# Performance work log

Measured on AMD Instinct MI355X. Metric: run time of the kernel, lower is better.

The kernel has to match this reference:

```python
import jax, jax.numpy as jnp
import numpy as np

LOSS_WEIGHT = 1.0
BIG = 1e9  # finite sentinel for masked-out pixels (avoids inf-grad NaNs)


def setup_inputs() -> dict:
    key = jax.random.key(0)
    k1, k2 = jax.random.split(key)
    B, N, H, W = 4, 6890, 64, 64
    vert2d = jax.random.uniform(k1, (B, N, 2), dtype=jnp.float32) * jnp.array([W, H], jnp.float32)
    mask = jax.random.randint(k2, (B, H, W), 0, 2, dtype=jnp.int32)
    return {"vert2d": vert2d, "mask": mask}


def reference(vert2d, mask):
    B, N, _ = vert2d.shape
    _, H, W = mask.shape
    scale = jnp.array([W, H], vert2d.dtype)
    v = vert2d / scale  # [B,N,2], normalized
    # all pixel coords as (x, y), normalized -- the dense equivalent of torch.where points
    ys, xs = jnp.meshgrid(jnp.arange(H), jnp.arange(W), indexing="ij")
    pts = (jnp.stack([xs.ravel(), ys.ravel()], axis=-1).astype(v.dtype) / scale)  # [HW,2]
    valid = (mask.reshape(B, -1) > 0)  # [B,HW] boolean membership of each pixel
    # pairwise L2 distances: [B,N,HW]
    diff = v[:, :, None, :] - pts[None, None, :, :]
    d = jnp.sqrt(jnp.sum(diff * diff, axis=-1))
    dm = jnp.where(valid[:, None, :], d, BIG)
    # sum over mask points of min over verts  +  sum over verts of min over mask points
    loss = jnp.sum(jnp.min(dm, axis=1) * valid) + jnp.sum(jnp.min(dm, axis=2))
    return LOSS_WEIGHT * loss
```

## Files before the change

### kernel.cpp

```cpp
#include <hip/hip_runtime.h>

#define NB 4
#define NV 6890
#define HW 4096
#define NPAD 6912
#define T1_CS 108
#define T1_BLOCKS 1024
#define T2_BLOCKS 896
#define NRED_BLOCKS 172

#define OFF_VT   0
#define OFF_PL   442368
#define OFF_T1   704512
#define OFF_T2   770048
#define OFF_PART 880640

#define FLT_MAX_BITS 0x7F7FFFFFu
#define FINF 3.402823466e38f
#define PBIG 1.0e18f

__global__ __launch_bounds__(256) void k_prep(const float* __restrict__ vert,
                                              const int* __restrict__ mask,
                                              float4* __restrict__ vt,
                                              float4* __restrict__ pl,
                                              unsigned* __restrict__ t1,
                                              unsigned* __restrict__ t2) {
    int gid = blockIdx.x * 256 + threadIdx.x;
    t2[gid] = FLT_MAX_BITS;
    int b = gid / NPAD, n = gid - b * NPAD;
    if (n < NV) {
        float2 v = reinterpret_cast<const float2*>(vert)[b * NV + n];
        vt[gid] = make_float4(-2.f * v.x, -2.f * v.y, fmaf(v.x, v.x, v.y * v.y), 0.f);
    } else {
        vt[gid] = make_float4(0.f, 0.f, PBIG, 0.f);
    }
    if (gid < NB * HW) {
        t1[gid] = FLT_MAX_BITS;
        float fx = (float)(gid & 63), fy = (float)((gid >> 6) & 63);
        float pz = (mask[gid] > 0) ? fmaf(fx, fx, fy * fy) : PBIG;
        pl[gid] = make_float4(-2.f * fx, -2.f * fy, pz, 0.f);
    }
}

__global__ __launch_bounds__(256) void k_main(const float* __restrict__ vert,
                                              const float4* __restrict__ vt,
                                              const float4* __restrict__ pl,
                                              unsigned* __restrict__ t1,
                                              unsigned* __restrict__ t2) {
    __shared__ float4 lds[128];
    int bx = blockIdx.x, tid = threadIdx.x;
    if (bx < T1_BLOCKS) {
        int c = bx & 63, q = (bx >> 6) & 3, b = bx >> 8;
        if (tid < T1_CS) lds[tid] = vt[b * NPAD + c * T1_CS + tid];
        __syncthreads();
        int x = tid & 63, ry = tid >> 6;
        float fx = (float)x;
        float fy0 = (float)(q * 16 + ry);
        float fy1 = fy0 + 4.f, fy2 = fy0 + 8.f, fy3 = fy0 + 12.f;
        float m0 = FINF, m1 = FINF, m2 = FINF, m3 = FINF;
        #pragma unroll 4
        for (int i = 0; i < T1_CS; i += 2) {
            float4 a = lds[i], g = lds[i + 1];
            float ta = fmaf(a.x, fx, a.z);
            float tg = fmaf(g.x, fx, g.z);
            m0 = fminf(m0, fminf(fmaf(a.y, fy0, ta), fmaf(g.y, fy0, tg)));
            m1 = fminf(m1, fminf(fmaf(a.y, fy1, ta), fmaf(g.y, fy1, tg)));
            m2 = fminf(m2, fminf(fmaf(a.y, fy2, ta), fmaf(g.y, fy2, tg)));
            m3 = fminf(m3, fminf(fmaf(a.y, fy3, ta), fmaf(g.y, fy3, tg)));
        }
        float fx2 = fx * fx;
        int y0 = q * 16 + ry;
        unsigned* tp = t1 + (b << 12) + x;
        m0 = fmaxf(fmaf(fy0, fy0, fx2) + m0, 0.f);
        m1 = fmaxf(fmaf(fy1, fy1, fx2) + m1, 0.f);
        m2 = fmaxf(fmaf(fy2, fy2, fx2) + m2, 0.f);
        m3 = fmaxf(fmaf(fy3, fy3, fx2) + m3, 0.f);
        atomicMin(tp + (y0     ) * 64, __float_as_uint(m0));
        atomicMin(tp + (y0 +  4) * 64, __float_as_uint(m1));
        atomicMin(tp + (y0 +  8) * 64, __float_as_uint(m2));
        atomicMin(tp + (y0 + 12) * 64, __float_as_uint(m3));
    } else {
        int t2i = bx - T1_BLOCKS;
        int pc = t2i & 31;
        int r  = t2i >> 5;
        int g  = r % 7, b = r / 7;
        if (tid < 128) lds[tid] = pl[b * HW + pc * 128 + tid];
        __syncthreads();
        int n0 = g * 1024 + tid;
        const float2* vv = reinterpret_cast<const float2*>(vert) + b * NV;
        float vx[4], vy[4];
        bool  val[4];
        #pragma unroll
        for (int k = 0; k < 4; ++k) {
            int n = n0 + 256 * k;
            val[k] = (n < NV);
            float2 t = val[k] ? vv[n] : make_float2(0.f, 0.f);
            vx[k] = t.x; vy[k] = t.y;
        }
        float mm[4] = {FINF, FINF, FINF, FINF};
        #pragma unroll 4
        for (int j = 0; j < 128; j += 2) {
            float4 a = lds[j], cc = lds[j + 1];
            #pragma unroll
            for (int k = 0; k < 4; ++k) {
                float da = fmaf(a.x,  vx[k], fmaf(a.y,  vy[k], a.z));
                float dc = fmaf(cc.x, vx[k], fmaf(cc.y, vy[k], cc.z));
                mm[k] = fminf(mm[k], fminf(da, dc));
            }
        }
        #pragma unroll
        for (int k = 0; k < 4; ++k) {
            if (val[k]) {
                float m = fmaxf(mm[k] + fmaf(vx[k], vx[k], vy[k] * vy[k]), 0.f);
                atomicMin(&t2[b * NPAD + n0 + 256 * k], __float_as_uint(m));
            }
        }
    }
}

__global__ __launch_bounds__(256) void k_red1(const unsigned* __restrict__ t1,
                                              const unsigned* __restrict__ t2,
                                              const int* __restrict__ mask,
                                              float* __restrict__ part) {
    int gid = blockIdx.x * 256 + threadIdx.x;
    float v = 0.f;
    if (gid < HW * NB) {
        if (mask[gid] > 0)
            v = sqrtf(__uint_as_float(t1[gid])) * (1.0f / 64.0f);
    } else {
        int j = gid - HW * NB;
        int bb = j / NPAD;
        int n  = j - bb * NPAD;
        if (n < NV)
            v = sqrtf(__uint_as_float(t2[j])) * (1.0f / 64.0f);
    }
    __shared__ float sbuf[4];
    for (int off = 32; off; off >>= 1) v += __shfl_down(v, off, 64);
    int lane = threadIdx.x & 63, wid = threadIdx.x >> 6;
    if (!lane) sbuf[wid] = v;
    __syncthreads();
    if (wid == 0) {
        v = (lane < 4) ? sbuf[lane] : 0.f;
        v += __shfl_down(v, 2, 64);
        v += __shfl_down(v, 1, 64);
        if (!lane) part[blockIdx.x] = v;
    }
}

__global__ __launch_bounds__(256) void k_red2(const float* __restrict__ part,
                                              float* __restrict__ out) {
    float v = (threadIdx.x < NRED_BLOCKS) ? part[threadIdx.x] : 0.f;
    __shared__ float sbuf[4];
    for (int off = 32; off; off >>= 1) v += __shfl_down(v, off, 64);
    int lane = threadIdx.x & 63, wid = threadIdx.x >> 6;
    if (!lane) sbuf[wid] = v;
    __syncthreads();
    if (threadIdx.x == 0) out[0] = sbuf[0] + sbuf[1] + sbuf[2] + sbuf[3];
}

extern "C" void kernel_launch(void* const* d_in, const int* in_sizes, int n_in,
                              void* d_out, int out_size, void* d_ws, size_t ws_size,
                              hipStream_t stream) {
    const float* vert = (const float*)d_in[0];
    const int*   mask = (const int*)d_in[1];
    char* ws = (char*)d_ws;
    float4*   vt  = (float4*)(ws + OFF_VT);
    float4*   pl  = (float4*)(ws + OFF_PL);
    unsigned* t1  = (unsigned*)(ws + OFF_T1);
    unsigned* t2  = (unsigned*)(ws + OFF_T2);
    float*    prt = (float*)(ws + OFF_PART);
    float*    out = (float*)d_out;

    k_prep<<<108, 256, 0, stream>>>(vert, mask, vt, pl, t1, t2);
    k_main<<<T1_BLOCKS + T2_BLOCKS, 256, 0, stream>>>(vert, vt, pl, t1, t2);
    k_red1<<<NRED_BLOCKS, 256, 0, stream>>>(t1, t2, mask, prt);
    k_red2<<<1, 256, 0, stream>>>(prt, out);
}
```

Baseline: 76.04 us.

## Fuse prep into main kernel, replace atomics with partial buffers, single-pass reduction

Removes the separate prep kernel by computing the vertex and pixel LDS tiles inside the main kernel, and doubles the per-block chunk sizes. Cross-block atomicMin is replaced by writing per-chunk partial minima to large scratch buffers, which the reduction kernel then min-reduces. The final sum uses an atomicAdd with a ticket counter so the second reduction kernel is no longer needed. This cuts two launches and the atomic contention, at the cost of more global memory traffic for the partial buffers and fewer blocks in the main kernel.

```diff
diff --git a/kernel.cpp b/kernel.cpp
--- a/kernel.cpp
+++ b/kernel.cpp
@@ -4,87 +4,75 @@
 #define NV 6890
 #define HW 4096
 #define NPAD 6912
-#define T1_CS 108
-#define T1_BLOCKS 1024
-#define T2_BLOCKS 896
+#define C1 32
+#define T1CS 216
+#define C2 16
+#define T1_BLOCKS 512
+#define T2_BLOCKS 448
 #define NRED_BLOCKS 172
 
-#define OFF_VT   0
-#define OFF_PL   442368
-#define OFF_T1   704512
-#define OFF_T2   770048
-#define OFF_PART 880640
+#define OFF_T1P 0
+#define OFF_T2P 2097152
+#define OFF_SUM 3866624
+#define OFF_TKT 3866628
 
-#define FLT_MAX_BITS 0x7F7FFFFFu
 #define FINF 3.402823466e38f
 #define PBIG 1.0e18f
 
-__global__ __launch_bounds__(256) void k_prep(const float* __restrict__ vert,
+__global__ __launch_bounds__(256) void k_main(const float* __restrict__ vert,
                                               const int* __restrict__ mask,
-                                              float4* __restrict__ vt,
-                                              float4* __restrict__ pl,
-                                              unsigned* __restrict__ t1,
-                                              unsigned* __restrict__ t2) {
-    int gid = blockIdx.x * 256 + threadIdx.x;
-    t2[gid] = FLT_MAX_BITS;
-    int b = gid / NPAD, n = gid - b * NPAD;
-    if (n < NV) {
-        float2 v = reinterpret_cast<const float2*>(vert)[b * NV + n];
-        vt[gid] = make_float4(-2.f * v.x, -2.f * v.y, fmaf(v.x, v.x, v.y * v.y), 0.f);
-    } else {
-        vt[gid] = make_float4(0.f, 0.f, PBIG, 0.f);
-    }
-    if (gid < NB * HW) {
-        t1[gid] = FLT_MAX_BITS;
-        float fx = (float)(gid & 63), fy = (float)((gid >> 6) & 63);
-        float pz = (mask[gid] > 0) ? fmaf(fx, fx, fy * fy) : PBIG;
-        pl[gid] = make_float4(-2.f * fx, -2.f * fy, pz, 0.f);
-    }
-}
-
-__global__ __launch_bounds__(256) void k_main(const float* __restrict__ vert,
-                                              const float4* __restrict__ vt,
-                                              const float4* __restrict__ pl,
-                                              unsigned* __restrict__ t1,
-                                              unsigned* __restrict__ t2) {
-    __shared__ float4 lds[128];
+                                              float* __restrict__ t1p,
+                                              float* __restrict__ t2p,
+                                              float* __restrict__ sum,
+                                              unsigned* __restrict__ tkt) {
+    __shared__ float4 lds[256];
     int bx = blockIdx.x, tid = threadIdx.x;
+    if (bx == 0 && tid == 0) { *sum = 0.f; *tkt = 0u; }
     if (bx < T1_BLOCKS) {
-        int c = bx & 63, q = (bx >> 6) & 3, b = bx >> 8;
-        if (tid < T1_CS) lds[tid] = vt[b * NPAD + c * T1_CS + tid];
+        int c = bx & 31, q = (bx >> 5) & 3, b = bx >> 7;
+        if (tid < T1CS) {
+            int n = c * T1CS + tid;
+            float4 w = make_float4(0.f, 0.f, PBIG, 0.f);
+            if (n < NV) {
+                float2 v = reinterpret_cast<const float2*>(vert)[b * NV + n];
+                w = make_float4(-2.f * v.x, -2.f * v.y, fmaf(v.x, v.x, v.y * v.y), 0.f);
+            }
+            lds[tid] = w;
+        }
         __syncthreads();
         int x = tid & 63, ry = tid >> 6;
-        float fx = (float)x;
+        float fx  = (float)x;
         float fy0 = (float)(q * 16 + ry);
         float fy1 = fy0 + 4.f, fy2 = fy0 + 8.f, fy3 = fy0 + 12.f;
         float m0 = FINF, m1 = FINF, m2 = FINF, m3 = FINF;
         #pragma unroll 4
-        for (int i = 0; i < T1_CS; i += 2) {
-            float4 a = lds[i], g = lds[i + 1];
-            float ta = fmaf(a.x, fx, a.z);
-            float tg = fmaf(g.x, fx, g.z);
-            m0 = fminf(m0, fminf(fmaf(a.y, fy0, ta), fmaf(g.y, fy0, tg)));
-            m1 = fminf(m1, fminf(fmaf(a.y, fy1, ta), fmaf(g.y, fy1, tg)));
-            m2 = fminf(m2, fminf(fmaf(a.y, fy2, ta), fmaf(g.y, fy2, tg)));
-            m3 = fminf(m3, fminf(fmaf(a.y, fy3, ta), fmaf(g.y, fy3, tg)));
+        for (int i = 0; i < T1CS; i += 2) {
+            float4 a = lds[i], g2 = lds[i + 1];
+            float ta = fmaf(a.x,  fx, a.z);
+            float tg = fmaf(g2.x, fx, g2.z);
+            m0 = fminf(m0, fminf(fmaf(a.y, fy0, ta), fmaf(g2.y, fy0, tg)));
+            m1 = fminf(m1, fminf(fmaf(a.y, fy1, ta), fmaf(g2.y, fy1, tg)));
+            m2 = fminf(m2, fminf(fmaf(a.y, fy2, ta), fmaf(g2.y, fy2, tg)));
+            m3 = fminf(m3, fminf(fmaf(a.y, fy3, ta), fmaf(g2.y, fy3, tg)));
         }
         float fx2 = fx * fx;
         int y0 = q * 16 + ry;
-        unsigned* tp = t1 + (b << 12) + x;
-        m0 = fmaxf(fmaf(fy0, fy0, fx2) + m0, 0.f);
-        m1 = fmaxf(fmaf(fy1, fy1, fx2) + m1, 0.f);
-        m2 = fmaxf(fmaf(fy2, fy2, fx2) + m2, 0.f);
-        m3 = fmaxf(fmaf(fy3, fy3, fx2) + m3, 0.f);
-        atomicMin(tp + (y0     ) * 64, __float_as_uint(m0));
-        atomicMin(tp + (y0 +  4) * 64, __float_as_uint(m1));
-        atomicMin(tp + (y0 +  8) * 64, __float_as_uint(m2));
-        atomicMin(tp + (y0 + 12) * 64, __float_as_uint(m3));
+        float* tp = t1p + ((c * NB + b) << 12) + x;
+        tp[(y0     ) * 64] = fmaf(fy0, fy0, fx2) + m0;
+        tp[(y0 +  4) * 64] = fmaf(fy1, fy1, fx2) + m1;
+        tp[(y0 +  8) * 64] = fmaf(fy2, fy2, fx2) + m2;
+        tp[(y0 + 12) * 64] = fmaf(fy3, fy3, fx2) + m3;
     } else {
         int t2i = bx - T1_BLOCKS;
-        int pc = t2i & 31;
-        int r  = t2i >> 5;
+        int pc = t2i & 15;
+        int r  = t2i >> 4;
         int g  = r % 7, b = r / 7;
-        if (tid < 128) lds[tid] = pl[b * HW + pc * 128 + tid];
+        {
+            int pix = pc * 256 + tid;
+            float fx = (float)(pix & 63), fy = (float)(pix >> 6);
+            float pz = (mask[b * HW + pix] > 0) ? fmaf(fx, fx, fy * fy) : PBIG;
+            lds[tid] = make_float4(-2.f * fx, -2.f * fy, pz, 0.f);
+        }
         __syncthreads();
         int n0 = g * 1024 + tid;
         const float2* vv = reinterpret_cast<const float2*>(vert) + b * NV;
@@ -98,8 +86,8 @@
             vx[k] = t.x; vy[k] = t.y;
         }
         float mm[4] = {FINF, FINF, FINF, FINF};
-        #pragma unroll 4
-        for (int j = 0; j < 128; j += 2) {
+        #pragma unroll 2
+        for (int j = 0; j < 256; j += 2) {
             float4 a = lds[j], cc = lds[j + 1];
             #pragma unroll
             for (int k = 0; k < 4; ++k) {
@@ -108,54 +96,55 @@
                 mm[k] = fminf(mm[k], fminf(da, dc));
             }
         }
+        float* op = t2p + pc * (NB * NPAD) + b * NPAD + n0;
         #pragma unroll
-        for (int k = 0; k < 4; ++k) {
-            if (val[k]) {
-                float m = fmaxf(mm[k] + fmaf(vx[k], vx[k], vy[k] * vy[k]), 0.f);
-                atomicMin(&t2[b * NPAD + n0 + 256 * k], __float_as_uint(m));
-            }
-        }
+        for (int k = 0; k < 4; ++k)
+            if (val[k]) op[256 * k] = mm[k] + fmaf(vx[k], vx[k], vy[k] * vy[k]);
     }
 }
 
-__global__ __launch_bounds__(256) void k_red1(const unsigned* __restrict__ t1,
-                                              const unsigned* __restrict__ t2,
-                                              const int* __restrict__ mask,
-                                              float* __restrict__ part) {
+__global__ __launch_bounds__(256) void k_red(const float* __restrict__ t1p,
+                                             const float* __restrict__ t2p,
+                                             const int* __restrict__ mask,
+                                             float* __restrict__ sum,
+                                             unsigned* __restrict__ tkt,
+                                             float* __restrict__ out) {
     int gid = blockIdx.x * 256 + threadIdx.x;
     float v = 0.f;
-    if (gid < HW * NB) {
-        if (mask[gid] > 0)
-            v = sqrtf(__uint_as_float(t1[gid])) * (1.0f / 64.0f);
+    if (gid < NB * HW) {
+        if (mask[gid] > 0) {
+            float m = FINF;
+            #pragma unroll
+            for (int c = 0; c < C1; ++c) m = fminf(m, t1p[c * (NB * HW) + gid]);
+            v = sqrtf(fmaxf(m, 0.f)) * (1.0f / 64.0f);
+        }
     } else {
-        int j = gid - HW * NB;
-        int bb = j / NPAD;
-        int n  = j - bb * NPAD;
-        if (n < NV)
-            v = sqrtf(__uint_as_float(t2[j])) * (1.0f / 64.0f);
+        int j = gid - NB * HW;
+        int b = j / NPAD;
+        int n = j - b * NPAD;
+        if (n < NV) {
+            float m = FINF;
+            #pragma unroll
+            for (int pc = 0; pc < C2; ++pc) m = fminf(m, t2p[pc * (NB * NPAD) + j]);
+            v = sqrtf(fmaxf(m, 0.f)) * (1.0f / 64.0f);
+        }
     }
     __shared__ float sbuf[4];
+    __shared__ bool last;
     for (int off = 32; off; off >>= 1) v += __shfl_down(v, off, 64);
     int lane = threadIdx.x & 63, wid = threadIdx.x >> 6;
     if (!lane) sbuf[wid] = v;
     __syncthreads();
-    if (wid == 0) {
-        v = (lane < 4) ? sbuf[lane] : 0.f;
-        v += __shfl_down(v, 2, 64);
-        v += __shfl_down(v, 1, 64);
-        if (!lane) part[blockIdx.x] = v;
+    if (threadIdx.x == 0) {
+        float bs = sbuf[0] + sbuf[1] + sbuf[2] + sbuf[3];
+        atomicAdd(sum, bs);
+        __threadfence();
+        unsigned t = atomicAdd(tkt, 1u);
+        last = (t == NRED_BLOCKS - 1);
     }
-}
-
-__global__ __launch_bounds__(256) void k_red2(const float* __restrict__ part,
-                                              float* __restrict__ out) {
-    float v = (threadIdx.x < NRED_BLOCKS) ? part[threadIdx.x] : 0.f;
-    __shared__ float sbuf[4];
-    for (int off = 32; off; off >>= 1) v += __shfl_down(v, off, 64);
-    int lane = threadIdx.x & 63, wid = threadIdx.x >> 6;
-    if (!lane) sbuf[wid] = v;
     __syncthreads();
-    if (threadIdx.x == 0) out[0] = sbuf[0] + sbuf[1] + sbuf[2] + sbuf[3];
+    if (last && threadIdx.x == 0)
+        out[0] = atomicAdd(sum, 0.f);
 }
 
 extern "C" void kernel_launch(void* const* d_in, const int* in_sizes, int n_in,
@@ -164,15 +153,12 @@
     const float* vert = (const float*)d_in[0];
     const int*   mask = (const int*)d_in[1];
     char* ws = (char*)d_ws;
-    float4*   vt  = (float4*)(ws + OFF_VT);
-    float4*   pl  = (float4*)(ws + OFF_PL);
-    unsigned* t1  = (unsigned*)(ws + OFF_T1);
-    unsigned* t2  = (unsigned*)(ws + OFF_T2);
-    float*    prt = (float*)(ws + OFF_PART);
+    float*    t1p = (float*)(ws + OFF_T1P);
+    float*    t2p = (float*)(ws + OFF_T2P);
+    float*    sum = (float*)(ws + OFF_SUM);
+    unsigned* tkt = (unsigned*)(ws + OFF_TKT);
     float*    out = (float*)d_out;
 
-    k_prep<<<108, 256, 0, stream>>>(vert, mask, vt, pl, t1, t2);
-    k_main<<<T1_BLOCKS + T2_BLOCKS, 256, 0, stream>>>(vert, vt, pl, t1, t2);
-    k_red1<<<NRED_BLOCKS, 256, 0, stream>>>(t1, t2, mask, prt);
-    k_red2<<<1, 256, 0, stream>>>(prt, out);
+    k_main<<<T1_BLOCKS + T2_BLOCKS, 256, 0, stream>>>(vert, mask, t1p, t2p, sum, tkt);
+    k_red <<<NRED_BLOCKS, 256, 0, stream>>>(t1p, t2p, mask, sum, tkt, out);
 }
```

Result: slower. 79.92 us (+5.1%).
